# Performance work log

Measured on AMD Instinct MI355X. Metric: run time of the kernel, lower is better.

The kernel has to match this reference:

```python
import math
import jax, jax.numpy as jnp
import numpy as np

WS = 8   # window_size
SS = 4   # shift_size
HEADS = 8
C = 256
B = 8
HH = 128
WW = 128


def _cpb_table_np(ws):
    # relative coords table: [(2ws-1)*(2ws-1), 2], log-spaced
    ch = np.arange(-(ws - 1), ws, dtype=np.float32)
    cw = np.arange(-(ws - 1), ws, dtype=np.float32)
    gh, gw = np.meshgrid(ch, cw, indexing='ij')
    t = np.stack([gh, gw], axis=-1).reshape(-1, 2)
    t = t / float(ws - 1)
    t = t * 8.0
    t = np.sign(t) * np.log2(np.abs(t) + 1.0) / math.log2(8)
    return t.astype(np.float32)


def _rel_pos_index_np(ws):
    ch = np.arange(ws)
    cw = np.arange(ws)
    gh, gw = np.meshgrid(ch, cw, indexing='ij')
    cf = np.stack([gh.reshape(-1), gw.reshape(-1)])  # [2, N]
    rel = cf[:, :, None] - cf[:, None, :]            # [2, N, N]
    rel = rel.transpose(1, 2, 0).astype(np.int64)
    rel[:, :, 0] += ws - 1
    rel[:, :, 1] += ws - 1
    rel[:, :, 0] *= 2 * ws - 1
    return rel.sum(-1)  # [N, N]


def _shift_mask_np(H, W, ws, ss):
    img = np.zeros((H, W), dtype=np.float32)
    cnt = 0
    for hs in (slice(0, -ws), slice(-ws, -ss), slice(-ss, None)):
        for wsl in (slice(0, -ws), slice(-ws, -ss), slice(-ss, None)):
            img[hs, wsl] = cnt
            cnt += 1
    nH, nW = H // ws, W // ws
    mw = img.reshape(nH, ws, nW, ws).transpose(0, 2, 1, 3).reshape(-1, ws * ws)  # [nWin, N]
    diff = mw[:, None, :] - mw[:, :, None]
    return np.where(diff != 0, -100.0, 0.0).astype(np.float32)  # [nWin, N, N]


def setup_inputs() -> dict:
    key = jax.random.key(0)
    ks = jax.random.split(key, 6)
    return {
        'x': jax.random.normal(ks[0], (B, HH * WW, C), dtype=jnp.float32),
        'qkv_w': jax.random.normal(ks[1], (3 * C, C), dtype=jnp.float32) * 0.02,
        'q_bias': jnp.zeros((C,), dtype=jnp.float32),
        'v_bias': jnp.zeros((C,), dtype=jnp.float32),
        'logit_scale': jnp.log(10.0 * jnp.ones((HEADS, 1, 1), dtype=jnp.float32)),
        'cpb_w1': jax.random.normal(ks[2], (512, 2), dtype=jnp.float32) * 0.02,
        'cpb_b1': jnp.zeros((512,), dtype=jnp.float32),
        'cpb_w2': jax.random.normal(ks[3], (HEADS, 512), dtype=jnp.float32) * 0.02,
        'proj_w': jax.random.normal(ks[4], (C, C), dtype=jnp.float32) * 0.02,
        'proj_b': jnp.zeros((C,), dtype=jnp.float32),
        'H': HH,
        'W': WW,
    }


def reference(x, qkv_w, q_bias, v_bias, logit_scale, cpb_w1, cpb_b1, cpb_w2,
              proj_w, proj_b, H, W):
    Bsz, L, Cd = x.shape
    heads = cpb_w2.shape[0]
    hd = Cd // heads
    N = WS * WS
    nH, nW = H // WS, W // WS
    nWin = nH * nW

    # shift + window partition
    xi = x.reshape(Bsz, H, W, Cd)
    xi = jnp.roll(xi, (-SS, -SS), axis=(1, 2))
    xw = xi.reshape(Bsz, nH, WS, nW, WS, Cd).transpose(0, 1, 3, 2, 4, 5)
    xw = xw.reshape(Bsz * nWin, N, Cd)  # [B_, N, C]

    # qkv with zeroed k-bias
    qkv_bias = jnp.concatenate([q_bias, jnp.zeros_like(v_bias), v_bias])
    qkv = xw @ qkv_w.T + qkv_bias  # [B_, N, 3C]
    qkv = qkv.reshape(Bsz * nWin, N, 3, heads, hd).transpose(2, 0, 3, 1, 4)
    q, k, v = qkv[0], qkv[1], qkv[2]  # [B_, h, N, d]

    # cosine attention
    qn = q / jnp.maximum(jnp.linalg.norm(q, axis=-1, keepdims=True), 1e-12)
    kn = k / jnp.maximum(jnp.linalg.norm(k, axis=-1, keepdims=True), 1e-12)
    attn = jnp.einsum('bhnd,bhmd->bhnm', qn, kn)
    scale = jnp.exp(jnp.minimum(logit_scale, math.log(1.0 / 0.01)))  # [h,1,1]
    attn = attn * scale[None]

    # log-CPB relative position bias
    table = jnp.asarray(_cpb_table_np(WS))                     # [(2W-1)^2, 2]
    hid = jax.nn.relu(table @ cpb_w1.T + cpb_b1)               # [T, 512]
    bias_table = hid @ cpb_w2.T                                # [T, h]
    rel_idx = jnp.asarray(_rel_pos_index_np(WS))               # [N, N]
    bias = bias_table[rel_idx.reshape(-1)].reshape(N, N, heads)
    bias = 16.0 * jax.nn.sigmoid(bias).transpose(2, 0, 1)      # [h, N, N]
    attn = attn + bias[None]

    # shift mask
    mask = jnp.asarray(_shift_mask_np(H, W, WS, SS))           # [nWin, N, N]
    attn = attn.reshape(Bsz, nWin, heads, N, N) + mask[None, :, None]
    attn = attn.reshape(Bsz * nWin, heads, N, N)

    attn = jax.nn.softmax(attn, axis=-1)
    out = jnp.einsum('bhnm,bhmd->bhnd', attn, v)
    out = out.transpose(0, 2, 1, 3).reshape(Bsz * nWin, N, Cd)
    out = out @ proj_w.T + proj_b

    # window reverse + unshift
    out = out.reshape(Bsz, nH, nW, WS, WS, Cd).transpose(0, 1, 3, 2, 4, 5)
    out = out.reshape(Bsz, H, W, Cd)
    out = jnp.roll(out, (SS, SS), axis=(1, 2))
    return out.reshape(Bsz, L, Cd)
```

## Files before the change

kernel.cpp:

```cpp
#include <hip/hip_runtime.h>
#include <cstdint>
#include <cstddef>

typedef short bf16x8 __attribute__((ext_vector_type(8)));
typedef float f32x4 __attribute__((ext_vector_type(4)));


#define WS_QKVW   0u
#define WS_PROJW  393216u
#define WS_QKVB   524288u
#define WS_SCALE  527360u
#define WS_BT     527392u
#define WS_BIAS   534592u

#define XS_US   0
#define QK_US   16896
#define VS_US   57856
#define SMEM_US 76288
#define SMEM_BYTES (SMEM_US * 2)

__device__ __forceinline__ unsigned short f2b(float f) {
  union { float f; unsigned int u; } v; v.f = f;
  return (unsigned short)((v.u + 0x7FFFu + ((v.u >> 16) & 1u)) >> 16);
}
__device__ __forceinline__ float b2f(unsigned short h) {
  union { unsigned int u; float f; } v; v.u = ((unsigned int)h) << 16;
  return v.f;
}


__global__ void prep_weights(const float* __restrict__ qkv_w,
                             const float* __restrict__ q_bias,
                             const float* __restrict__ v_bias,
                             const float* __restrict__ logit_scale,
                             const float* __restrict__ proj_w,
                             unsigned char* __restrict__ ws) {
  int gid = blockIdx.x * 256 + threadIdx.x;
  unsigned short* qw = (unsigned short*)(ws + WS_QKVW);
  unsigned short* pw = (unsigned short*)(ws + WS_PROJW);
  if (gid < 196608) qw[gid] = f2b(qkv_w[gid]);
  if (gid < 65536)  pw[gid] = f2b(proj_w[gid]);
  if (gid < 768) {
    float v = 0.f;
    if (gid < 256) v = q_bias[gid];
    else if (gid >= 512) v = v_bias[gid - 512];
    ((float*)(ws + WS_QKVB))[gid] = v;
  }
  if (gid < 8) {
    float ls = logit_scale[gid];
    ((float*)(ws + WS_SCALE))[gid] = __expf(fminf(ls, 4.605170185988091f));
  }
}

__global__ void prep_cpb(const float* __restrict__ w1, const float* __restrict__ b1,
                         const float* __restrict__ w2, unsigned char* __restrict__ ws) {
  __shared__ float hid[512];
  const int r = blockIdx.x;
  const int dh = r / 15, dw = r % 15;
  float t0 = ((float)(dh - 7)) / 7.0f * 8.0f;
  float t1 = ((float)(dw - 7)) / 7.0f * 8.0f;
  float a0 = log2f(fabsf(t0) + 1.0f) / 3.0f;
  float a1 = log2f(fabsf(t1) + 1.0f) / 3.0f;
  t0 = (t0 < 0.f) ? -a0 : a0;
  t1 = (t1 < 0.f) ? -a1 : a1;
  const int j = threadIdx.x;
  float h = t0 * w1[2 * j] + t1 * w1[2 * j + 1] + b1[j];
  hid[j] = fmaxf(h, 0.f);
  __syncthreads();
  const int wave = j >> 6, lane = j & 63;
  float p = 0.f;
  for (int jj = lane; jj < 512; jj += 64) p += hid[jj] * w2[wave * 512 + jj];
  #pragma unroll
  for (int off = 32; off > 0; off >>= 1) p += __shfl_down(p, off, 64);
  if (lane == 0) ((float*)(ws + WS_BT))[r * 8 + wave] = p;
}

__global__ void prep_bias(unsigned char* __restrict__ ws) {
  int u = blockIdx.x * 256 + threadIdx.x;
  int reg = u & 3;
  int lane = (u >> 2) & 63;
  int nt = (u >> 8) & 3;
  int mt = (u >> 10) & 3;
  int h = (u >> 12);
  int i = mt * 16 + (lane >> 4) * 4 + reg;
  int jx = nt * 16 + (lane & 15);
  int idx = ((i >> 3) - (jx >> 3) + 7) * 15 + ((i & 7) - (jx & 7) + 7);
  float xv = ((const float*)(ws + WS_BT))[idx * 8 + h];
  ((float*)(ws + WS_BIAS))[u] = 16.0f / (1.0f + __expf(-xv));
}


__launch_bounds__(512, 2)
__global__ void swin_main(const float* __restrict__ x,
                          const unsigned char* __restrict__ ws,
                          float* __restrict__ out,
                          const float* __restrict__ proj_b) {
  extern __shared__ unsigned short sm[];
  const int tid = threadIdx.x;
  const int wave = tid >> 6;
  const int lane = tid & 63;
  const int quad = lane >> 4;
  const int l15 = lane & 15;

  const int blk = blockIdx.x;
  const int b = blk >> 8;
  const int win = blk & 255;
  const int wr = win >> 4;
  const int wc = win & 15;

  const unsigned short* qkvw = (const unsigned short*)(ws + WS_QKVW);
  const unsigned short* projw = (const unsigned short*)(ws + WS_PROJW);
  const float* qkvb = (const float*)(ws + WS_QKVB);
  const float* scales = (const float*)(ws + WS_SCALE);
  const float* bias_sw = (const float*)(ws + WS_BIAS);

  {
    const int t = tid >> 3;
    const int cg = tid & 7;
    const int rw = t >> 3, cw = t & 7;
    const int gr = (wr * 8 + rw + 4) & 127;
    const int gc = (wc * 8 + cw + 4) & 127;
    const float* src = x + ((size_t)b * 16384 + gr * 128 + gc) * 256 + cg * 32;
    unsigned short* dst = sm + XS_US + t * 264 + cg * 32;
    #pragma unroll
    for (int kk = 0; kk < 4; ++kk) {
      f32x4 a = *(const f32x4*)(src + kk * 8);
      f32x4 c = *(const f32x4*)(src + kk * 8 + 4);
      union { bf16x8 v; unsigned short u[8]; } pk;
      #pragma unroll
      for (int e = 0; e < 4; ++e) { pk.u[e] = f2b(a[e]); pk.u[4 + e] = f2b(c[e]); }
      *(bf16x8*)(dst + kk * 8) = pk.v;
    }
  }
  __syncthreads();

  {
    f32x4 acc[4][6];
    #pragma unroll
    for (int mt = 0; mt < 4; ++mt)
      #pragma unroll
      for (int nt = 0; nt < 6; ++nt) acc[mt][nt] = f32x4{0.f, 0.f, 0.f, 0.f};
    const int ncol0 = wave * 96;
    for (int k0 = 0; k0 < 256; k0 += 32) {
      bf16x8 afr[4];
      #pragma unroll
      for (int mt = 0; mt < 4; ++mt)
        afr[mt] = *(const bf16x8*)(sm + XS_US + (mt * 16 + l15) * 264 + k0 + quad * 8);
      #pragma unroll
      for (int nt = 0; nt < 6; ++nt) {
        const int n = ncol0 + nt * 16 + l15;
        bf16x8 bfr = *(const bf16x8*)(qkvw + n * 256 + k0 + quad * 8);
        #pragma unroll
        for (int mt = 0; mt < 4; ++mt)
          acc[mt][nt] = __builtin_amdgcn_mfma_f32_16x16x32_bf16(afr[mt], bfr, acc[mt][nt], 0, 0, 0);
      }
    }
    #pragma unroll
    for (int nt = 0; nt < 6; ++nt) {
      const int n0 = ncol0 + nt * 16;
      const float bias = qkvb[n0 + l15];
      const int which = n0 >> 8;
      const int head = (n0 & 255) >> 5;
      const int chan = (n0 & 31) + l15;
      #pragma unroll
      for (int mt = 0; mt < 4; ++mt) {
        const int tok0 = mt * 16 + quad * 4;
        if (which == 2) {
          union { unsigned short u[4]; unsigned long long ll; } pk;
          #pragma unroll
          for (int r = 0; r < 4; ++r) pk.u[r] = f2b(acc[mt][nt][r] + bias);
          *(unsigned long long*)(sm + VS_US + head * 2304 + chan * 72 + tok0) = pk.ll;
        } else {
          unsigned short* q = sm + QK_US + head * 5120 + which * 2560 + chan;
          #pragma unroll
          for (int r = 0; r < 4; ++r) q[(tok0 + r) * 40] = f2b(acc[mt][nt][r] + bias);
        }
      }
    }
  }
  __syncthreads();

  {
    #pragma unroll
    for (int it = 0; it < 2; ++it) {
      const int task = tid + it * 512;
      const int isk = task >> 9;
      const int rem = task & 511;
      const int head = rem >> 6;
      const int tok = rem & 63;
      unsigned short* p = sm + QK_US + head * 5120 + isk * 2560 + tok * 40;
      float vals[32];
      float ss = 0.f;
      #pragma unroll
      for (int c8 = 0; c8 < 4; ++c8) {
        bf16x8 vv = *(const bf16x8*)(p + c8 * 8);
        #pragma unroll
        for (int e = 0; e < 8; ++e) {
          float f = b2f((unsigned short)vv[e]);
          vals[c8 * 8 + e] = f;
          ss += f * f;
        }
      }
      float inv = 1.0f / fmaxf(sqrtf(ss), 1e-12f);
      if (isk == 0) inv *= scales[head];
      #pragma unroll
      for (int c8 = 0; c8 < 4; ++c8) {
        union { bf16x8 v; unsigned short u[8]; } pk;
        #pragma unroll
        for (int e = 0; e < 8; ++e) pk.u[e] = f2b(vals[c8 * 8 + e] * inv);
        *(bf16x8*)(p + c8 * 8) = pk.v;
      }
    }
  }
  __syncthreads();

  float rinv[4][4];
  f32x4 o[4][2];
  {
    const int h = wave;
    const unsigned short* qb = sm + QK_US + h * 5120;
    const unsigned short* kb = qb + 2560;
    f32x4 s[4][4];
    bf16x8 aq[4];
    #pragma unroll
    for (int mt = 0; mt < 4; ++mt)
      aq[mt] = *(const bf16x8*)(qb + (mt * 16 + l15) * 40 + quad * 8);
    #pragma unroll
    for (int nt = 0; nt < 4; ++nt) {
      bf16x8 bk = *(const bf16x8*)(kb + (nt * 16 + l15) * 40 + quad * 8);
      #pragma unroll
      for (int mt = 0; mt < 4; ++mt)
        s[mt][nt] = __builtin_amdgcn_mfma_f32_16x16x32_bf16(aq[mt], bk, f32x4{0.f, 0.f, 0.f, 0.f}, 0, 0, 0);
    }
    const bool has_mask = (wr == 15) || (wc == 15);
    #pragma unroll
    for (int mt = 0; mt < 4; ++mt) {
      #pragma unroll
      for (int nt = 0; nt < 4; ++nt) {
        f32x4 bv = *(const f32x4*)(bias_sw + (size_t)(((h * 4 + mt) * 4 + nt) * 64 + lane) * 4);
        #pragma unroll
        for (int r = 0; r < 4; ++r) s[mt][nt][r] += bv[r];
        if (has_mask) {
          const int j = nt * 16 + l15;
          const int brj = (wr == 15) ? (((j >> 3) < 4) ? 1 : 2) : 0;
          const int bcj = (wc == 15) ? (((j & 7) < 4) ? 1 : 2) : 0;
          #pragma unroll
          for (int r = 0; r < 4; ++r) {
            const int i = mt * 16 + quad * 4 + r;
            const int bri = (wr == 15) ? (((i >> 3) < 4) ? 1 : 2) : 0;
            const int bci = (wc == 15) ? (((i & 7) < 4) ? 1 : 2) : 0;
            if (bri != brj || bci != bcj) s[mt][nt][r] -= 100.0f;
          }
        }
      }
    }
    #pragma unroll
    for (int mt = 0; mt < 4; ++mt) {
      #pragma unroll
      for (int r = 0; r < 4; ++r) {
        float m = fmaxf(fmaxf(s[mt][0][r], s[mt][1][r]), fmaxf(s[mt][2][r], s[mt][3][r]));
        #pragma unroll
        for (int off = 1; off < 16; off <<= 1) m = fmaxf(m, __shfl_xor(m, off, 64));
        float sum = 0.f;
        #pragma unroll
        for (int nt = 0; nt < 4; ++nt) {
          float p = __expf(s[mt][nt][r] - m);
          s[mt][nt][r] = p;
          sum += p;
        }
        #pragma unroll
        for (int off = 1; off < 16; off <<= 1) sum += __shfl_xor(sum, off, 64);
        rinv[mt][r] = 1.0f / sum;
      }
    }
    unsigned short* pbuf = sm + QK_US + h * 5120;
    #pragma unroll
    for (int mt = 0; mt < 4; ++mt) {
      #pragma unroll
      for (int r = 0; r < 4; ++r) {
        const int row = mt * 16 + quad * 4 + r;
        #pragma unroll
        for (int nt = 0; nt < 4; ++nt)
          pbuf[row * 72 + nt * 16 + l15] = f2b(s[mt][nt][r]);
      }
    }
    __syncthreads();
    #pragma unroll
    for (int mt = 0; mt < 4; ++mt)
      #pragma unroll
      for (int nc = 0; nc < 2; ++nc) o[mt][nc] = f32x4{0.f, 0.f, 0.f, 0.f};
    const unsigned short* vb = sm + VS_US + h * 2304;
    #pragma unroll
    for (int ks = 0; ks < 2; ++ks) {
      bf16x8 ap[4];
      #pragma unroll
      for (int mt = 0; mt < 4; ++mt)
        ap[mt] = *(const bf16x8*)(pbuf + (mt * 16 + l15) * 72 + ks * 32 + quad * 8);
      #pragma unroll
      for (int nc = 0; nc < 2; ++nc) {
        bf16x8 bv = *(const bf16x8*)(vb + (nc * 16 + l15) * 72 + ks * 32 + quad * 8);
        #pragma unroll
        for (int mt = 0; mt < 4; ++mt)
          o[mt][nc] = __builtin_amdgcn_mfma_f32_16x16x32_bf16(ap[mt], bv, o[mt][nc], 0, 0, 0);
      }
    }
    #pragma unroll
    for (int mt = 0; mt < 4; ++mt) {
      #pragma unroll
      for (int nc = 0; nc < 2; ++nc) {
        #pragma unroll
        for (int r = 0; r < 4; ++r) {
          const int tok = mt * 16 + quad * 4 + r;
          sm[XS_US + tok * 264 + h * 32 + nc * 16 + l15] = f2b(o[mt][nc][r] * rinv[mt][r]);
        }
      }
    }
  }
  __syncthreads();

  {
    f32x4 acc[4][2];
    #pragma unroll
    for (int mt = 0; mt < 4; ++mt)
      #pragma unroll
      for (int nt = 0; nt < 2; ++nt) acc[mt][nt] = f32x4{0.f, 0.f, 0.f, 0.f};
    const int ncol0 = wave * 32;
    for (int k0 = 0; k0 < 256; k0 += 32) {
      bf16x8 afr[4];
      #pragma unroll
      for (int mt = 0; mt < 4; ++mt)
        afr[mt] = *(const bf16x8*)(sm + XS_US + (mt * 16 + l15) * 264 + k0 + quad * 8);
      #pragma unroll
      for (int nt = 0; nt < 2; ++nt) {
        const int n = ncol0 + nt * 16 + l15;
        bf16x8 bfr = *(const bf16x8*)(projw + n * 256 + k0 + quad * 8);
        #pragma unroll
        for (int mt = 0; mt < 4; ++mt)
          acc[mt][nt] = __builtin_amdgcn_mfma_f32_16x16x32_bf16(afr[mt], bfr, acc[mt][nt], 0, 0, 0);
      }
    }
    #pragma unroll
    for (int nt = 0; nt < 2; ++nt) {
      const int col = ncol0 + nt * 16 + l15;
      const float pb = proj_b[col];
      #pragma unroll
      for (int mt = 0; mt < 4; ++mt) {
        #pragma unroll
        for (int r = 0; r < 4; ++r) {
          const int tok = mt * 16 + quad * 4 + r;
          const int rw = tok >> 3, cw = tok & 7;
          const int gr = (wr * 8 + rw + 4) & 127;
          const int gc = (wc * 8 + cw + 4) & 127;
          out[((size_t)b * 16384 + gr * 128 + gc) * 256 + col] = acc[mt][nt][r] + pb;
        }
      }
    }
  }
}


extern "C" void kernel_launch(void* const* d_in, const int* in_sizes, int n_in,
                              void* d_out, int out_size, void* d_ws, size_t ws_size,
                              hipStream_t stream) {
  const float* x           = (const float*)d_in[0];
  const float* qkv_w       = (const float*)d_in[1];
  const float* q_bias      = (const float*)d_in[2];
  const float* v_bias      = (const float*)d_in[3];
  const float* logit_scale = (const float*)d_in[4];
  const float* cpb_w1      = (const float*)d_in[5];
  const float* cpb_b1      = (const float*)d_in[6];
  const float* cpb_w2      = (const float*)d_in[7];
  const float* proj_w      = (const float*)d_in[8];
  const float* proj_b      = (const float*)d_in[9];
  unsigned char* ws = (unsigned char*)d_ws;
  float* out = (float*)d_out;

  prep_weights<<<768, 256, 0, stream>>>(qkv_w, q_bias, v_bias, logit_scale, proj_w, ws);
  prep_cpb<<<225, 512, 0, stream>>>(cpb_w1, cpb_b1, cpb_w2, ws);
  prep_bias<<<128, 256, 0, stream>>>(ws);

  (void)hipFuncSetAttribute((const void*)swin_main,
                            hipFuncAttributeMaxDynamicSharedMemorySize, SMEM_BYTES);
  swin_main<<<2048, 512, SMEM_BYTES, stream>>>(x, ws, out, proj_b);
}
```

Baseline: 491.4 us.

## Fuse per-head QKV, normalization and attention per wave with compact LDS

```diff
diff --git a/kernel.cpp b/kernel.cpp
--- a/kernel.cpp
+++ b/kernel.cpp
@@ -14,9 +14,8 @@
 #define WS_BIAS   534592u
 
 #define XS_US   0
-#define QK_US   16896
-#define VS_US   57856
-#define SMEM_US 76288
+#define SCR_US  16896
+#define SMEM_US (16896 + 8 * 2560)
 #define SMEM_BYTES (SMEM_US * 2)
 
 __device__ __forceinline__ unsigned short f2b(float f) {
@@ -79,18 +78,18 @@
   int u = blockIdx.x * 256 + threadIdx.x;
   int reg = u & 3;
   int lane = (u >> 2) & 63;
-  int nt = (u >> 8) & 3;
-  int mt = (u >> 10) & 3;
+  int it = (u >> 8) & 3;
+  int jt = (u >> 10) & 3;
   int h = (u >> 12);
-  int i = mt * 16 + (lane >> 4) * 4 + reg;
-  int jx = nt * 16 + (lane & 15);
+  int i = it * 16 + (lane & 15);
+  int jx = jt * 16 + (lane >> 4) * 4 + reg;
   int idx = ((i >> 3) - (jx >> 3) + 7) * 15 + ((i & 7) - (jx & 7) + 7);
   float xv = ((const float*)(ws + WS_BT))[idx * 8 + h];
   ((float*)(ws + WS_BIAS))[u] = 16.0f / (1.0f + __expf(-xv));
 }
 
 
-__launch_bounds__(512, 2)
+__launch_bounds__(512, 4)
 __global__ void swin_main(const float* __restrict__ x,
                           const unsigned char* __restrict__ ws,
                           float* __restrict__ out,
@@ -134,188 +133,238 @@
   }
   __syncthreads();
 
+  const int h = wave;
+  unsigned short* buf = sm + SCR_US + wave * 2560;
+  const float sc = scales[h];
+
+  bf16x8 qfr[4], kfr[4];
+
   {
-    f32x4 acc[4][6];
-    #pragma unroll
-    for (int mt = 0; mt < 4; ++mt)
-      #pragma unroll
-      for (int nt = 0; nt < 6; ++nt) acc[mt][nt] = f32x4{0.f, 0.f, 0.f, 0.f};
-    const int ncol0 = wave * 96;
+    f32x4 accq[4][2], acck[4][2];
+    #pragma unroll
+    for (int mt = 0; mt < 4; ++mt)
+      #pragma unroll
+      for (int n2 = 0; n2 < 2; ++n2) {
+        accq[mt][n2] = f32x4{0.f, 0.f, 0.f, 0.f};
+        acck[mt][n2] = f32x4{0.f, 0.f, 0.f, 0.f};
+      }
     for (int k0 = 0; k0 < 256; k0 += 32) {
       bf16x8 afr[4];
       #pragma unroll
       for (int mt = 0; mt < 4; ++mt)
         afr[mt] = *(const bf16x8*)(sm + XS_US + (mt * 16 + l15) * 264 + k0 + quad * 8);
       #pragma unroll
-      for (int nt = 0; nt < 6; ++nt) {
-        const int n = ncol0 + nt * 16 + l15;
-        bf16x8 bfr = *(const bf16x8*)(qkvw + n * 256 + k0 + quad * 8);
+      for (int n2 = 0; n2 < 2; ++n2) {
+        const bf16x8 wq = *(const bf16x8*)(qkvw + (size_t)(32 * h + n2 * 16 + l15) * 256 + k0 + quad * 8);
+        const bf16x8 wk = *(const bf16x8*)(qkvw + (size_t)(256 + 32 * h + n2 * 16 + l15) * 256 + k0 + quad * 8);
+        #pragma unroll
+        for (int mt = 0; mt < 4; ++mt) {
+          accq[mt][n2] = __builtin_amdgcn_mfma_f32_16x16x32_bf16(afr[mt], wq, accq[mt][n2], 0, 0, 0);
+          acck[mt][n2] = __builtin_amdgcn_mfma_f32_16x16x32_bf16(afr[mt], wk, acck[mt][n2], 0, 0, 0);
+        }
+      }
+    }
+    const float bq0 = qkvb[32 * h + l15];
+    const float bq1 = qkvb[32 * h + 16 + l15];
+    #pragma unroll
+    for (int mt = 0; mt < 4; ++mt) {
+      f32x4 ss;
+      #pragma unroll
+      for (int r = 0; r < 4; ++r) {
+        float a0 = accq[mt][0][r] + bq0;
+        float a1 = accq[mt][1][r] + bq1;
+        accq[mt][0][r] = a0; accq[mt][1][r] = a1;
+        ss[r] = a0 * a0 + a1 * a1;
+      }
+      #pragma unroll
+      for (int off = 1; off < 16; off <<= 1)
+        #pragma unroll
+        for (int r = 0; r < 4; ++r) ss[r] += __shfl_xor(ss[r], off, 64);
+      #pragma unroll
+      for (int r = 0; r < 4; ++r) {
+        const float inv = sc / fmaxf(sqrtf(ss[r]), 1e-12f);
+        accq[mt][0][r] *= inv; accq[mt][1][r] *= inv;
+      }
+    }
+    #pragma unroll
+    for (int mt = 0; mt < 4; ++mt) {
+      f32x4 ss;
+      #pragma unroll
+      for (int r = 0; r < 4; ++r) {
+        float a0 = acck[mt][0][r], a1 = acck[mt][1][r];
+        ss[r] = a0 * a0 + a1 * a1;
+      }
+      #pragma unroll
+      for (int off = 1; off < 16; off <<= 1)
+        #pragma unroll
+        for (int r = 0; r < 4; ++r) ss[r] += __shfl_xor(ss[r], off, 64);
+      #pragma unroll
+      for (int r = 0; r < 4; ++r) {
+        const float inv = 1.0f / fmaxf(sqrtf(ss[r]), 1e-12f);
+        acck[mt][0][r] *= inv; acck[mt][1][r] *= inv;
+      }
+    }
+    #pragma unroll
+    for (int mt = 0; mt < 4; ++mt)
+      #pragma unroll
+      for (int n2 = 0; n2 < 2; ++n2)
+        #pragma unroll
+        for (int r = 0; r < 4; ++r)
+          buf[(mt * 16 + quad * 4 + r) * 40 + n2 * 16 + l15] = f2b(accq[mt][n2][r]);
+    #pragma unroll
+    for (int mt = 0; mt < 4; ++mt)
+      qfr[mt] = *(const bf16x8*)(buf + (mt * 16 + l15) * 40 + quad * 8);
+    #pragma unroll
+    for (int mt = 0; mt < 4; ++mt)
+      #pragma unroll
+      for (int n2 = 0; n2 < 2; ++n2)
+        #pragma unroll
+        for (int r = 0; r < 4; ++r)
+          buf[(mt * 16 + quad * 4 + r) * 40 + n2 * 16 + l15] = f2b(acck[mt][n2][r]);
+    #pragma unroll
+    for (int mt = 0; mt < 4; ++mt)
+      kfr[mt] = *(const bf16x8*)(buf + (mt * 16 + l15) * 40 + quad * 8);
+  }
+
+  {
+    f32x4 accv[4][2];
+    #pragma unroll
+    for (int mt = 0; mt < 4; ++mt)
+      #pragma unroll
+      for (int n2 = 0; n2 < 2; ++n2) accv[mt][n2] = f32x4{0.f, 0.f, 0.f, 0.f};
+    for (int k0 = 0; k0 < 256; k0 += 32) {
+      bf16x8 afr[4];
+      #pragma unroll
+      for (int mt = 0; mt < 4; ++mt)
+        afr[mt] = *(const bf16x8*)(sm + XS_US + (mt * 16 + l15) * 264 + k0 + quad * 8);
+      #pragma unroll
+      for (int n2 = 0; n2 < 2; ++n2) {
+        const bf16x8 wv = *(const bf16x8*)(qkvw + (size_t)(512 + 32 * h + n2 * 16 + l15) * 256 + k0 + quad * 8);
         #pragma unroll
         for (int mt = 0; mt < 4; ++mt)
-          acc[mt][nt] = __builtin_amdgcn_mfma_f32_16x16x32_bf16(afr[mt], bfr, acc[mt][nt], 0, 0, 0);
-      }
-    }
-    #pragma unroll
-    for (int nt = 0; nt < 6; ++nt) {
-      const int n0 = ncol0 + nt * 16;
-      const float bias = qkvb[n0 + l15];
-      const int which = n0 >> 8;
-      const int head = (n0 & 255) >> 5;
-      const int chan = (n0 & 31) + l15;
-      #pragma unroll
-      for (int mt = 0; mt < 4; ++mt) {
-        const int tok0 = mt * 16 + quad * 4;
-        if (which == 2) {
+          accv[mt][n2] = __builtin_amdgcn_mfma_f32_16x16x32_bf16(afr[mt], wv, accv[mt][n2], 0, 0, 0);
+      }
+    }
+    const float bv0 = qkvb[512 + 32 * h + l15];
+    const float bv1 = qkvb[512 + 32 * h + 16 + l15];
+    #pragma unroll
+    for (int mt = 0; mt < 4; ++mt)
+      #pragma unroll
+      for (int n2 = 0; n2 < 2; ++n2) {
+        const float bb = n2 ? bv1 : bv0;
+        union { unsigned short u[4]; unsigned long long ll; } pk;
+        #pragma unroll
+        for (int r = 0; r < 4; ++r) pk.u[r] = f2b(accv[mt][n2][r] + bb);
+        *(unsigned long long*)(buf + (n2 * 16 + l15) * 72 + mt * 16 + quad * 4) = pk.ll;
+      }
+  }
+
+  f32x4 o[4][2];
+  {
+    f32x4 st[4][4];
+    #pragma unroll
+    for (int jt = 0; jt < 4; ++jt)
+      #pragma unroll
+      for (int it = 0; it < 4; ++it)
+        st[jt][it] = __builtin_amdgcn_mfma_f32_16x16x32_bf16(kfr[jt], qfr[it], f32x4{0.f, 0.f, 0.f, 0.f}, 0, 0, 0);
+
+    const bool has_mask = (wr == 15) || (wc == 15);
+    const float* bsw = bias_sw + (size_t)h * 4096 + (size_t)lane * 4;
+    #pragma unroll
+    for (int jt = 0; jt < 4; ++jt) {
+      #pragma unroll
+      for (int it = 0; it < 4; ++it) {
+        f32x4 bv = *(const f32x4*)(bsw + (jt * 4 + it) * 256);
+        #pragma unroll
+        for (int r = 0; r < 4; ++r) st[jt][it][r] += bv[r];
+        if (has_mask) {
+          const int i = it * 16 + l15;
+          const int bri = (wr == 15) ? (((i >> 3) < 4) ? 1 : 2) : 0;
+          const int bci = (wc == 15) ? (((i & 7) < 4) ? 1 : 2) : 0;
+          #pragma unroll
+          for (int r = 0; r < 4; ++r) {
+            const int j = jt * 16 + quad * 4 + r;
+            const int brj = (wr == 15) ? (((j >> 3) < 4) ? 1 : 2) : 0;
+            const int bcj = (wc == 15) ? (((j & 7) < 4) ? 1 : 2) : 0;
+            if (bri != brj || bci != bcj) st[jt][it][r] -= 100.0f;
+          }
+        }
+      }
+    }
+
+    #pragma unroll
+    for (int it = 0; it < 4; ++it) {
+      f32x4 mm;
+      #pragma unroll
+      for (int r = 0; r < 4; ++r)
+        mm[r] = fmaxf(fmaxf(st[0][it][r], st[1][it][r]), fmaxf(st[2][it][r], st[3][it][r]));
+      float m = fmaxf(fmaxf(mm[0], mm[1]), fmaxf(mm[2], mm[3]));
+      m = fmaxf(m, __shfl_xor(m, 16, 64));
+      m = fmaxf(m, __shfl_xor(m, 32, 64));
+      f32x4 sv = f32x4{0.f, 0.f, 0.f, 0.f};
+      #pragma unroll
+      for (int jt = 0; jt < 4; ++jt)
+        #pragma unroll
+        for (int r = 0; r < 4; ++r) {
+          const float p = __expf(st[jt][it][r] - m);
+          st[jt][it][r] = p;
+          sv[r] += p;
+        }
+      float sum = (sv[0] + sv[1]) + (sv[2] + sv[3]);
+      sum += __shfl_xor(sum, 16, 64);
+      sum += __shfl_xor(sum, 32, 64);
+      const float rinv = 1.0f / sum;
+      #pragma unroll
+      for (int jt = 0; jt < 4; ++jt)
+        #pragma unroll
+        for (int r = 0; r < 4; ++r) st[jt][it][r] *= rinv;
+    }
+
+    bf16x8 vfr[2][2];
+    #pragma unroll
+    for (int ks = 0; ks < 2; ++ks)
+      #pragma unroll
+      for (int nc = 0; nc < 2; ++nc)
+        vfr[ks][nc] = *(const bf16x8*)(buf + (nc * 16 + l15) * 72 + ks * 32 + quad * 8);
+
+    #pragma unroll
+    for (int mt = 0; mt < 4; ++mt)
+      #pragma unroll
+      for (int nc = 0; nc < 2; ++nc) o[mt][nc] = f32x4{0.f, 0.f, 0.f, 0.f};
+
+    #pragma unroll
+    for (int ks = 0; ks < 2; ++ks) {
+      #pragma unroll
+      for (int it = 0; it < 4; ++it)
+        #pragma unroll
+        for (int jh = 0; jh < 2; ++jh) {
+          const int jt = ks * 2 + jh;
           union { unsigned short u[4]; unsigned long long ll; } pk;
           #pragma unroll
-          for (int r = 0; r < 4; ++r) pk.u[r] = f2b(acc[mt][nt][r] + bias);
-          *(unsigned long long*)(sm + VS_US + head * 2304 + chan * 72 + tok0) = pk.ll;
-        } else {
-          unsigned short* q = sm + QK_US + head * 5120 + which * 2560 + chan;
-          #pragma unroll
-          for (int r = 0; r < 4; ++r) q[(tok0 + r) * 40] = f2b(acc[mt][nt][r] + bias);
+          for (int r = 0; r < 4; ++r) pk.u[r] = f2b(st[jt][it][r]);
+          *(unsigned long long*)(buf + (it * 16 + l15) * 40 + jh * 16 + quad * 4) = pk.ll;
         }
-      }
-    }
-  }
+      bf16x8 pa[4];
+      #pragma unroll
+      for (int mt = 0; mt < 4; ++mt)
+        pa[mt] = *(const bf16x8*)(buf + (mt * 16 + l15) * 40 + quad * 8);
+      #pragma unroll
+      for (int nc = 0; nc < 2; ++nc)
+        #pragma unroll
+        for (int mt = 0; mt < 4; ++mt)
+          o[mt][nc] = __builtin_amdgcn_mfma_f32_16x16x32_bf16(pa[mt], vfr[ks][nc], o[mt][nc], 0, 0, 0);
+    }
+  }
+
   __syncthreads();
 
-  {
-    #pragma unroll
-    for (int it = 0; it < 2; ++it) {
-      const int task = tid + it * 512;
-      const int isk = task >> 9;
-      const int rem = task & 511;
-      const int head = rem >> 6;
-      const int tok = rem & 63;
-      unsigned short* p = sm + QK_US + head * 5120 + isk * 2560 + tok * 40;
-      float vals[32];
-      float ss = 0.f;
-      #pragma unroll
-      for (int c8 = 0; c8 < 4; ++c8) {
-        bf16x8 vv = *(const bf16x8*)(p + c8 * 8);
-        #pragma unroll
-        for (int e = 0; e < 8; ++e) {
-          float f = b2f((unsigned short)vv[e]);
-          vals[c8 * 8 + e] = f;
-          ss += f * f;
-        }
-      }
-      float inv = 1.0f / fmaxf(sqrtf(ss), 1e-12f);
-      if (isk == 0) inv *= scales[head];
-      #pragma unroll
-      for (int c8 = 0; c8 < 4; ++c8) {
-        union { bf16x8 v; unsigned short u[8]; } pk;
-        #pragma unroll
-        for (int e = 0; e < 8; ++e) pk.u[e] = f2b(vals[c8 * 8 + e] * inv);
-        *(bf16x8*)(p + c8 * 8) = pk.v;
-      }
-    }
-  }
-  __syncthreads();
-
-  float rinv[4][4];
-  f32x4 o[4][2];
-  {
-    const int h = wave;
-    const unsigned short* qb = sm + QK_US + h * 5120;
-    const unsigned short* kb = qb + 2560;
-    f32x4 s[4][4];
-    bf16x8 aq[4];
-    #pragma unroll
-    for (int mt = 0; mt < 4; ++mt)
-      aq[mt] = *(const bf16x8*)(qb + (mt * 16 + l15) * 40 + quad * 8);
-    #pragma unroll
-    for (int nt = 0; nt < 4; ++nt) {
-      bf16x8 bk = *(const bf16x8*)(kb + (nt * 16 + l15) * 40 + quad * 8);
-      #pragma unroll
-      for (int mt = 0; mt < 4; ++mt)
-        s[mt][nt] = __builtin_amdgcn_mfma_f32_16x16x32_bf16(aq[mt], bk, f32x4{0.f, 0.f, 0.f, 0.f}, 0, 0, 0);
-    }
-    const bool has_mask = (wr == 15) || (wc == 15);
-    #pragma unroll
-    for (int mt = 0; mt < 4; ++mt) {
-      #pragma unroll
-      for (int nt = 0; nt < 4; ++nt) {
-        f32x4 bv = *(const f32x4*)(bias_sw + (size_t)(((h * 4 + mt) * 4 + nt) * 64 + lane) * 4);
-        #pragma unroll
-        for (int r = 0; r < 4; ++r) s[mt][nt][r] += bv[r];
-        if (has_mask) {
-          const int j = nt * 16 + l15;
-          const int brj = (wr == 15) ? (((j >> 3) < 4) ? 1 : 2) : 0;
-          const int bcj = (wc == 15) ? (((j & 7) < 4) ? 1 : 2) : 0;
-          #pragma unroll
-          for (int r = 0; r < 4; ++r) {
-            const int i = mt * 16 + quad * 4 + r;
-            const int bri = (wr == 15) ? (((i >> 3) < 4) ? 1 : 2) : 0;
-            const int bci = (wc == 15) ? (((i & 7) < 4) ? 1 : 2) : 0;
-            if (bri != brj || bci != bcj) s[mt][nt][r] -= 100.0f;
-          }
-        }
-      }
-    }
-    #pragma unroll
-    for (int mt = 0; mt < 4; ++mt) {
-      #pragma unroll
-      for (int r = 0; r < 4; ++r) {
-        float m = fmaxf(fmaxf(s[mt][0][r], s[mt][1][r]), fmaxf(s[mt][2][r], s[mt][3][r]));
-        #pragma unroll
-        for (int off = 1; off < 16; off <<= 1) m = fmaxf(m, __shfl_xor(m, off, 64));
-        float sum = 0.f;
-        #pragma unroll
-        for (int nt = 0; nt < 4; ++nt) {
-          float p = __expf(s[mt][nt][r] - m);
-          s[mt][nt][r] = p;
-          sum += p;
-        }
-        #pragma unroll
-        for (int off = 1; off < 16; off <<= 1) sum += __shfl_xor(sum, off, 64);
-        rinv[mt][r] = 1.0f / sum;
-      }
-    }
-    unsigned short* pbuf = sm + QK_US + h * 5120;
-    #pragma unroll
-    for (int mt = 0; mt < 4; ++mt) {
-      #pragma unroll
-      for (int r = 0; r < 4; ++r) {
-        const int row = mt * 16 + quad * 4 + r;
-        #pragma unroll
-        for (int nt = 0; nt < 4; ++nt)
-          pbuf[row * 72 + nt * 16 + l15] = f2b(s[mt][nt][r]);
-      }
-    }
-    __syncthreads();
-    #pragma unroll
-    for (int mt = 0; mt < 4; ++mt)
-      #pragma unroll
-      for (int nc = 0; nc < 2; ++nc) o[mt][nc] = f32x4{0.f, 0.f, 0.f, 0.f};
-    const unsigned short* vb = sm + VS_US + h * 2304;
-    #pragma unroll
-    for (int ks = 0; ks < 2; ++ks) {
-      bf16x8 ap[4];
-      #pragma unroll
-      for (int mt = 0; mt < 4; ++mt)
-        ap[mt] = *(const bf16x8*)(pbuf + (mt * 16 + l15) * 72 + ks * 32 + quad * 8);
-      #pragma unroll
-      for (int nc = 0; nc < 2; ++nc) {
-        bf16x8 bv = *(const bf16x8*)(vb + (nc * 16 + l15) * 72 + ks * 32 + quad * 8);
-        #pragma unroll
-        for (int mt = 0; mt < 4; ++mt)
-          o[mt][nc] = __builtin_amdgcn_mfma_f32_16x16x32_bf16(ap[mt], bv, o[mt][nc], 0, 0, 0);
-      }
-    }
-    #pragma unroll
-    for (int mt = 0; mt < 4; ++mt) {
-      #pragma unroll
-      for (int nc = 0; nc < 2; ++nc) {
-        #pragma unroll
-        for (int r = 0; r < 4; ++r) {
-          const int tok = mt * 16 + quad * 4 + r;
-          sm[XS_US + tok * 264 + h * 32 + nc * 16 + l15] = f2b(o[mt][nc][r] * rinv[mt][r]);
-        }
-      }
-    }
-  }
+  #pragma unroll
+  for (int mt = 0; mt < 4; ++mt)
+    #pragma unroll
+    for (int nc = 0; nc < 2; ++nc)
+      #pragma unroll
+      for (int r = 0; r < 4; ++r)
+        sm[XS_US + (mt * 16 + quad * 4 + r) * 264 + h * 32 + nc * 16 + l15] = f2b(o[mt][nc][r]);
   __syncthreads();
 
   {
@@ -333,7 +382,7 @@
       #pragma unroll
       for (int nt = 0; nt < 2; ++nt) {
         const int n = ncol0 + nt * 16 + l15;
-        bf16x8 bfr = *(const bf16x8*)(projw + n * 256 + k0 + quad * 8);
+        bf16x8 bfr = *(const bf16x8*)(projw + (size_t)n * 256 + k0 + quad * 8);
         #pragma unroll
         for (int mt = 0; mt < 4; ++mt)
           acc[mt][nt] = __builtin_amdgcn_mfma_f32_16x16x32_bf16(afr[mt], bfr, acc[mt][nt], 0, 0, 0);
```

Result: faster. 405.4 us (-17.5%).
